# Kernel tuning notes

Measured on AMD Instinct MI355X. Metric: run time of the kernel, lower is better.

The kernel has to match this reference:

```python
import jax, jax.numpy as jnp
import numpy as np

DIM = 1024
NUM_HEADS = 16
HEAD_DIM = DIM // NUM_HEADS
EPS = 1e-5


def layernorm(x, scale, bias):
    # LayerNorm over the last (head_dim) axis
    mu = jnp.mean(x, axis=-1, keepdims=True)
    var = jnp.var(x, axis=-1, keepdims=True)
    return (x - mu) * jax.lax.rsqrt(var + EPS) * scale + bias


def rope(q):
    # q: [B, H, S, Hd]; standard rotate-half RoPE over head_dim
    S, Hd = q.shape[-2], q.shape[-1]
    inv_freq = 1.0 / (10000.0 ** (jnp.arange(0, Hd, 2, dtype=jnp.float32) / Hd))
    ang = jnp.arange(S, dtype=jnp.float32)[:, None] * inv_freq  # [S, Hd/2]
    cos, sin = jnp.cos(ang), jnp.sin(ang)
    q1, q2 = jnp.split(q, 2, axis=-1)
    return jnp.concatenate([q1 * cos - q2 * sin, q1 * sin + q2 * cos], axis=-1)


def setup_inputs() -> dict:
    key = jax.random.key(0)
    ks = jax.random.split(key, 8)
    B, S, S_ctx = 4, 2048, 2048
    s = 0.02
    return {
        "x": jax.random.normal(ks[0], (B, S, DIM), dtype=jnp.float32),
        "context": jax.random.normal(ks[1], (B, S_ctx, DIM), dtype=jnp.float32),
        "q_w": jax.random.normal(ks[2], (DIM, DIM), dtype=jnp.float32) * s,
        "kv_w": jax.random.normal(ks[3], (DIM, 2 * DIM), dtype=jnp.float32) * s,
        "qn_scale": jnp.ones((HEAD_DIM,), jnp.float32),
        "qn_bias": jnp.zeros((HEAD_DIM,), jnp.float32),
        "kn_scale": jnp.ones((HEAD_DIM,), jnp.float32),
        "kn_bias": jnp.zeros((HEAD_DIM,), jnp.float32),
        "proj_w": jax.random.normal(ks[4], (DIM, DIM), dtype=jnp.float32) * s,
        "proj_b": jnp.zeros((DIM,), jnp.float32),
    }


def reference(x, context, q_w, kv_w, qn_scale, qn_bias, kn_scale, kn_bias, proj_w, proj_b):
    B, S, C = x.shape
    S_ctx = context.shape[1]
    H, Hd = NUM_HEADS, HEAD_DIM
    # projections (no bias: qkv_bias=False)
    q = (x @ q_w).reshape(B, S, H, Hd).transpose(0, 2, 1, 3)        # [B,H,S,Hd]
    kv = (context @ kv_w).reshape(B, S_ctx, 2, H, Hd)
    k = kv[:, :, 0].transpose(0, 2, 1, 3)                           # [B,H,Sc,Hd]
    v = kv[:, :, 1].transpose(0, 2, 1, 3)
    # per-head LayerNorm on q and k
    q = layernorm(q, qn_scale, qn_bias)
    k = layernorm(k, kn_scale, kn_bias)
    # RoPE on q only (as in the original forward)
    q = rope(q)
    # SDPA (eval path: no mask, no dropout)
    scale = 1.0 / jnp.sqrt(jnp.float32(Hd))
    logits = jnp.einsum("bhsd,bhtd->bhst", q, k) * scale
    attn = jax.nn.softmax(logits, axis=-1)
    out = jnp.einsum("bhst,bhtd->bhsd", attn, v)                    # [B,H,S,Hd]
    out = out.transpose(0, 2, 1, 3).reshape(B, S, C)
    return out @ proj_w + proj_b
```

## Files before the change

kernel.cpp:

```cpp
#include <hip/hip_runtime.h>
#include <hip/hip_bf16.h>


typedef short bf16x8 __attribute__((ext_vector_type(8)));
typedef float f32x4 __attribute__((ext_vector_type(4)));

__device__ __forceinline__ short f2s(float f) {
    __hip_bfloat16 h = __float2bfloat16(f);
    return __builtin_bit_cast(short, h);
}

__device__ __forceinline__ f32x4 mfma16(bf16x8 a, bf16x8 b, f32x4 c) {
    return __builtin_amdgcn_mfma_f32_16x16x32_bf16(a, b, c, 0, 0, 0);
}

__device__ __forceinline__ void gload16(short* lds, const short* g) {
    __builtin_amdgcn_global_load_lds((const __attribute__((address_space(1))) void*)g,
                                     (__attribute__((address_space(3))) void*)lds,
                                     16, 0, 0);
}

__device__ __forceinline__ void drain_barrier() {
    asm volatile("s_waitcnt vmcnt(0) lgkmcnt(0)" ::: "memory");
    __syncthreads();
}

__device__ __forceinline__ unsigned int fbits(float f) {
    return __builtin_bit_cast(unsigned int, f);
}

__global__ __launch_bounds__(256) void conv_to_bf16(const float* __restrict__ x,
                                                    const float* __restrict__ ctx,
                                                    short* __restrict__ xb,
                                                    short* __restrict__ cb) {
    const size_t NV = 2097152;
    size_t i = (size_t)blockIdx.x * 256 + threadIdx.x;
    const float4* src = (i < NV) ? (const float4*)x : (const float4*)ctx;
    short* dst = (i < NV) ? xb : cb;
    size_t idx = (i < NV) ? i : i - NV;
    float4 v = src[idx];
    short4 o;
    o.x = f2s(v.x); o.y = f2s(v.y); o.z = f2s(v.z); o.w = f2s(v.w);
    ((short4*)dst)[idx] = o;
}

__global__ __launch_bounds__(256) void transpose_weights(
    const float* __restrict__ q_w, const float* __restrict__ kv_w,
    const float* __restrict__ proj_w,
    short* __restrict__ WqT, short* __restrict__ WkvT, short* __restrict__ WpT) {
    __shared__ float t[32][33];
    const float* src; short* dst; int ld, coff;
    switch (blockIdx.z) {
        case 0:  src = q_w;    dst = WqT;                 ld = 1024; coff = 0;    break;
        case 1:  src = kv_w;   dst = WkvT;                ld = 2048; coff = 0;    break;
        case 2:  src = kv_w;   dst = WkvT + 1024 * 1024;  ld = 2048; coff = 1024; break;
        default: src = proj_w; dst = WpT;                 ld = 1024; coff = 0;    break;
    }
    int n0 = blockIdx.x * 32, k0 = blockIdx.y * 32;
    int tx = threadIdx.x & 31, ty = threadIdx.x >> 5;
    #pragma unroll
    for (int j = 0; j < 32; j += 8)
        t[ty + j][tx] = src[(size_t)(k0 + ty + j) * ld + coff + n0 + tx];
    __syncthreads();
    #pragma unroll
    for (int j = 0; j < 32; j += 8)
        dst[(size_t)(n0 + ty + j) * 1024 + k0 + tx] = f2s(t[tx][ty + j]);
}

__global__ __launch_bounds__(256, 3) void gemm_qkv(
    const short* __restrict__ A,
    const short* __restrict__ Bt,
    const short* __restrict__ A2,
    const short* __restrict__ Bt2,
    const float* __restrict__ qn_scale, const float* __restrict__ qn_bias,
    const float* __restrict__ kn_scale, const float* __restrict__ kn_bias,
    short* __restrict__ outQ, short* __restrict__ outK, short* __restrict__ outV) {
    __shared__ short smem[24576];
    const int tid = threadIdx.x;
    const int w = tid >> 6, lane = tid & 63, quad = lane >> 4, l15 = lane & 15;
    const int wr = w & 1, wc = w >> 1;
    const int m0 = blockIdx.x * 128;

    const int y = blockIdx.y;
    const bool qpath = (y < 8);
    const int n0 = qpath ? y * 128 : (y - 8) * 128;
    const short* Ab = qpath ? A : A2;
    const short* Bb = qpath ? Bt : Bt2;
    const float* lns = qpath ? qn_scale : kn_scale;
    const float* lnb = qpath ? qn_bias : kn_bias;
    const bool vpath = (!qpath) && (n0 >= 1024);

    const int srow = lane >> 2, slot = lane & 3;
    const int kslot = (slot ^ ((srow >> 1) & 3)) * 8;
    const short* Ag0 = Ab + (size_t)(m0 + w * 32 + srow) * 1024 + kslot;
    const short* Ag1 = Ag0 + (size_t)16 * 1024;
    const short* Bg0 = Bb + (size_t)(n0 + w * 32 + srow) * 1024 + kslot;
    const short* Bg1 = Bg0 + (size_t)16 * 1024;
    short* Al = smem + w * 1024;
    short* Bl = smem + 4096 + w * 1024;

    f32x4 acc[4][4];
    #pragma unroll
    for (int r = 0; r < 4; r++)
        #pragma unroll
        for (int c = 0; c < 4; c++) acc[r][c] = f32x4{0.f, 0.f, 0.f, 0.f};

    const int rsw = (l15 >> 1) & 3;
    const int rch = (quad ^ rsw) * 8;

    gload16(Al,              Ag0);
    gload16(Al + 512,        Ag1);
    gload16(Bl,              Bg0);
    gload16(Bl + 512,        Bg1);
    gload16(Al + 8192,       Ag0 + 32);
    gload16(Al + 8192 + 512, Ag1 + 32);
    gload16(Bl + 8192,       Bg0 + 32);
    gload16(Bl + 8192 + 512, Bg1 + 32);
    asm volatile("s_waitcnt vmcnt(4) lgkmcnt(0)" ::: "memory");
    __builtin_amdgcn_s_barrier();

    int curo = 0;
    int pfo = 16384;
    #pragma unroll 1
    for (int t = 0; t < 32; t++) {
        if (t < 30) {
            const int k0 = (t + 2) * 32;
            gload16(Al + pfo,       Ag0 + k0);
            gload16(Al + pfo + 512, Ag1 + k0);
            gload16(Bl + pfo,       Bg0 + k0);
            gload16(Bl + pfo + 512, Bg1 + k0);
        }
        bf16x8 af[4], bfr[4];
        #pragma unroll
        for (int rt = 0; rt < 4; rt++)
            af[rt] = *(const bf16x8*)(smem + curo + (wr * 64 + rt * 16 + l15) * 32 + rch);
        #pragma unroll
        for (int ct = 0; ct < 4; ct++)
            bfr[ct] = *(const bf16x8*)(smem + curo + 4096 + (wc * 64 + ct * 16 + l15) * 32 + rch);
        #pragma unroll
        for (int rt = 0; rt < 4; rt++)
            #pragma unroll
            for (int ct = 0; ct < 4; ct++)
                acc[rt][ct] = mfma16(af[rt], bfr[ct], acc[rt][ct]);
        if (t < 30) {
            asm volatile("s_waitcnt vmcnt(4) lgkmcnt(0)" ::: "memory");
        } else {
            asm volatile("s_waitcnt vmcnt(0) lgkmcnt(0)" ::: "memory");
        }
        __builtin_amdgcn_s_barrier();
        curo += 8192; if (curo == 24576) curo = 0;
        pfo  += 8192; if (pfo  == 24576) pfo  = 0;
    }

    if (!vpath) {
        #pragma unroll
        for (int rt = 0; rt < 4; rt++) {
            #pragma unroll
            for (int i = 0; i < 4; i++) {
                float s = acc[rt][0][i] + acc[rt][1][i] + acc[rt][2][i] + acc[rt][3][i];
                float q = acc[rt][0][i] * acc[rt][0][i] + acc[rt][1][i] * acc[rt][1][i] +
                          acc[rt][2][i] * acc[rt][2][i] + acc[rt][3][i] * acc[rt][3][i];
                #pragma unroll
                for (int off = 1; off < 16; off <<= 1) {
                    s += __shfl_xor(s, off, 64);
                    q += __shfl_xor(q, off, 64);
                }
                float mu = s * (1.f / 64.f);
                float var = q * (1.f / 64.f) - mu * mu;
                float rs = rsqrtf(var + 1e-5f);
                float vals[4];
                #pragma unroll
                for (int ct = 0; ct < 4; ct++) {
                    int hd = ct * 16 + l15;
                    vals[ct] = (acc[rt][ct][i] - mu) * rs * lns[hd] + lnb[hd];
                }
                if (qpath) {
                    int sp = (m0 + wr * 64 + rt * 16 + quad * 4 + i) & 2047;
                    #pragma unroll
                    for (int ct = 0; ct < 2; ct++) {
                        int hd1 = ct * 16 + l15;
                        float ang = (float)sp * exp2f((float)hd1 * (-13.287712379549449f / 32.f));
                        float sn, cs;
                        sincosf(ang, &sn, &cs);
                        float v1 = vals[ct], v2 = vals[ct + 2];
                        vals[ct]     = v1 * cs - v2 * sn;
                        vals[ct + 2] = v1 * sn + v2 * cs;
                    }
                    #pragma unroll
                    for (int ct = 0; ct < 4; ct++) vals[ct] *= 0.1803368801f;
                }
                #pragma unroll
                for (int ct = 0; ct < 4; ct++) acc[rt][ct][i] = vals[ct];
            }
        }
        drain_barrier();
        short* Csm = smem;
        #pragma unroll
        for (int rt = 0; rt < 4; rt++)
            #pragma unroll
            for (int ct = 0; ct < 4; ct++)
                #pragma unroll
                for (int i = 0; i < 4; i++)
                    Csm[(wr * 64 + rt * 16 + quad * 4 + i) * 132 + wc * 64 + ct * 16 + l15] =
                        f2s(acc[rt][ct][i]);
        drain_barrier();
        short* dst = qpath ? outQ : outK;
        #pragma unroll
        for (int it = 0; it < 8; it++) {
            int row = it * 16 + (tid >> 4);
            int chunk = tid & 15;
            bf16x8 v = *(const bf16x8*)(Csm + row * 132 + chunk * 8);
            int hh = ((n0 & 1023) >> 6) + (chunk >> 3);
            int m = m0 + row, b = m >> 11, sp = m & 2047;
            *(bf16x8*)(dst + ((size_t)(b * 16 + hh) * 2048 + sp) * 64 + (chunk & 7) * 8) = v;
        }
    } else {
        const int b = m0 >> 11, h = ((n0 - 1024) >> 6) + wc;
        const int sp = (m0 & 2047) + wr * 64 + quad * 4;
        #pragma unroll
        for (int rt = 0; rt < 4; rt++)
            #pragma unroll
            for (int ct = 0; ct < 4; ct++) {
                short4 pk;
                pk.x = f2s(acc[rt][ct][0]); pk.y = f2s(acc[rt][ct][1]);
                pk.z = f2s(acc[rt][ct][2]); pk.w = f2s(acc[rt][ct][3]);
                int hd = ct * 16 + l15;
                *(short4*)(outV + ((size_t)(b * 16 + h) * 64 + hd) * 2048 + sp + rt * 16) = pk;
            }
    }
}

__global__ __launch_bounds__(256, 4) void gemm_proj(
    const short* __restrict__ A,
    const short* __restrict__ Bt,
    float* __restrict__ outF,
    const float* __restrict__ bias_vec) {
    __shared__ short smem[18432];
    const int tid = threadIdx.x;
    const int w = tid >> 6, lane = tid & 63, quad = lane >> 4, l15 = lane & 15;
    const int wr = w & 1, wc = w >> 1;
    const int m0 = blockIdx.x * 64, n0 = blockIdx.y * 128;

    const int srow = lane >> 2, slot = lane & 3;
    const int kslot = (slot ^ ((srow >> 1) & 3)) * 8;
    const short* Ag0 = A + (size_t)(m0 + w * 16 + srow) * 1024 + kslot;
    const short* Bg0 = Bt + (size_t)(n0 + w * 32 + srow) * 1024 + kslot;
    const short* Bg1 = Bg0 + (size_t)16 * 1024;
    short* Al = smem + w * 512;
    short* Bl = smem + 2048 + w * 1024;

    f32x4 acc[2][4];
    #pragma unroll
    for (int r = 0; r < 2; r++)
        #pragma unroll
        for (int c = 0; c < 4; c++) acc[r][c] = f32x4{0.f, 0.f, 0.f, 0.f};

    const int rsw = (l15 >> 1) & 3;
    const int rch = (quad ^ rsw) * 8;

    gload16(Al,              Ag0);
    gload16(Bl,              Bg0);
    gload16(Bl + 512,        Bg1);
    gload16(Al + 6144,       Ag0 + 32);
    gload16(Bl + 6144,       Bg0 + 32);
    gload16(Bl + 6144 + 512, Bg1 + 32);
    asm volatile("s_waitcnt vmcnt(3) lgkmcnt(0)" ::: "memory");
    __builtin_amdgcn_s_barrier();

    int curo = 0;
    int pfo = 12288;
    #pragma unroll 1
    for (int t = 0; t < 32; t++) {
        if (t < 30) {
            const int k0 = (t + 2) * 32;
            gload16(Al + pfo,       Ag0 + k0);
            gload16(Bl + pfo,       Bg0 + k0);
            gload16(Bl + pfo + 512, Bg1 + k0);
        }
        bf16x8 af[2], bfr[4];
        #pragma unroll
        for (int rt = 0; rt < 2; rt++)
            af[rt] = *(const bf16x8*)(smem + curo + (wr * 32 + rt * 16 + l15) * 32 + rch);
        #pragma unroll
        for (int ct = 0; ct < 4; ct++)
            bfr[ct] = *(const bf16x8*)(smem + curo + 2048 + (wc * 64 + ct * 16 + l15) * 32 + rch);
        #pragma unroll
        for (int rt = 0; rt < 2; rt++)
            #pragma unroll
            for (int ct = 0; ct < 4; ct++)
                acc[rt][ct] = mfma16(af[rt], bfr[ct], acc[rt][ct]);
        if (t < 30) {
            asm volatile("s_waitcnt vmcnt(3) lgkmcnt(0)" ::: "memory");
        } else {
            asm volatile("s_waitcnt vmcnt(0) lgkmcnt(0)" ::: "memory");
        }
        __builtin_amdgcn_s_barrier();
        curo += 6144; if (curo == 18432) curo = 0;
        pfo  += 6144; if (pfo  == 18432) pfo  = 0;
    }

    #pragma unroll
    for (int rt = 0; rt < 2; rt++)
        #pragma unroll
        for (int i = 0; i < 4; i++) {
            size_t m = m0 + wr * 32 + rt * 16 + quad * 4 + i;
            #pragma unroll
            for (int ct = 0; ct < 4; ct++) {
                int n = n0 + wc * 64 + ct * 16 + l15;
                outF[m * 1024 + n] = acc[rt][ct][i] + bias_vec[n];
            }
        }
}

__global__ __launch_bounds__(512, 4) void attn_kernel(
    const short* __restrict__ Q,
    const short* __restrict__ K,
    const short* __restrict__ V,
    short* __restrict__ AO) {
    __shared__ short smem[8192 + 8192 + 8 * 32 * 72];
    const int tid = threadIdx.x;
    const int w = tid >> 6, lane = tid & 63, quad = lane >> 4, l15 = lane & 15;
    const int bh = blockIdx.x, qt = blockIdx.y;
    const short* Qb = Q + (size_t)bh * 2048 * 64;
    const short* Kb = K + (size_t)bh * 2048 * 64;
    const short* Vb = V + (size_t)bh * 64 * 2048;
    short* Pw = smem + 16384 + w * 2304;
    const int q0 = qt * 256 + w * 32;

    const int srow = lane >> 2, slot = lane & 3;
    const int sw = (slot ^ ((srow >> 1) & 3)) * 8;
    const int ws = w & 3;
    const bool kstager = (w < 4);
    const short* Sg = kstager ? (Kb + (size_t)(ws * 16 + srow) * 64 + sw)
                              : (Vb + (size_t)(ws * 16 + srow) * 2048 + sw);
    short* Sl0 = smem + (kstager ? 0 : 8192) + ws * 512;
    const int sstep = kstager ? 4096 : 64;

    bf16x8 bq[2][2];
    #pragma unroll
    for (int nt = 0; nt < 2; nt++)
        #pragma unroll
        for (int ks = 0; ks < 2; ks++)
            bq[nt][ks] = *(const bf16x8*)(Qb + (size_t)(q0 + nt * 16 + l15) * 64 + ks * 32 + quad * 8);

    f32x4 acco[4][2];
    #pragma unroll
    for (int ct = 0; ct < 4; ct++)
        #pragma unroll
        for (int nt = 0; nt < 2; nt++) acco[ct][nt] = f32x4{0.f, 0.f, 0.f, 0.f};
    float lsum[2] = {0.f, 0.f};
    const int rsw = (l15 >> 1) & 3;
    const int rch = (quad ^ rsw) * 8;

    gload16(Sl0,        Sg);
    gload16(Sl0 + 2048, Sg + 32);
    drain_barrier();

    #pragma unroll 1
    for (int t = 0; t < 32; t++) {
        const int cur = (t & 1) * 4096;
        if (t < 31) {
            const int nxt = 4096 - cur;
            gload16(Sl0 + nxt,        Sg + (t + 1) * sstep);
            gload16(Sl0 + nxt + 2048, Sg + (t + 1) * sstep + 32);
        }
        bf16x8 ak[4][2];
        #pragma unroll
        for (int mt = 0; mt < 4; mt++)
            #pragma unroll
            for (int ks = 0; ks < 2; ks++)
                ak[mt][ks] = *(const bf16x8*)(smem + cur + ks * 2048 + (mt * 16 + l15) * 32 + rch);

        #pragma unroll
        for (int mt = 0; mt < 4; mt++) {
            #pragma unroll
            for (int nt = 0; nt < 2; nt++) {
                f32x4 st = f32x4{0.f, 0.f, 0.f, 0.f};
                st = mfma16(ak[mt][0], bq[nt][0], st);
                st = mfma16(ak[mt][1], bq[nt][1], st);
                float e0 = __builtin_amdgcn_exp2f(st[0]);
                float e1 = __builtin_amdgcn_exp2f(st[1]);
                float e2 = __builtin_amdgcn_exp2f(st[2]);
                float e3 = __builtin_amdgcn_exp2f(st[3]);
                lsum[nt] += (e0 + e1) + (e2 + e3);
                unsigned int p01 = __builtin_amdgcn_perm(fbits(e1), fbits(e0), 0x07060302u);
                unsigned int p23 = __builtin_amdgcn_perm(fbits(e3), fbits(e2), 0x07060302u);
                uint2 pw;
                pw.x = p01; pw.y = p23;
                *(uint2*)(Pw + (nt * 16 + l15) * 72 + mt * 16 + quad * 4) = pw;
            }
        }
        asm volatile("" ::: "memory");

        bf16x8 av[4][2];
        #pragma unroll
        for (int ct = 0; ct < 4; ct++)
            #pragma unroll
            for (int ks = 0; ks < 2; ks++)
                av[ct][ks] = *(const bf16x8*)(smem + 8192 + cur + ks * 2048 + (ct * 16 + l15) * 32 + rch);

        bf16x8 bp[2][2];
        #pragma unroll
        for (int nt = 0; nt < 2; nt++)
            #pragma unroll
            for (int ks = 0; ks < 2; ks++)
                bp[nt][ks] = *(const bf16x8*)(Pw + (nt * 16 + l15) * 72 + ks * 32 + quad * 8);
        #pragma unroll
        for (int ct = 0; ct < 4; ct++)
            #pragma unroll
            for (int nt = 0; nt < 2; nt++)
                #pragma unroll
                for (int ks = 0; ks < 2; ks++)
                    acco[ct][nt] = mfma16(av[ct][ks], bp[nt][ks], acco[ct][nt]);
        drain_barrier();
    }

    #pragma unroll
    for (int nt = 0; nt < 2; nt++) {
        lsum[nt] += __shfl_xor(lsum[nt], 16, 64);
        lsum[nt] += __shfl_xor(lsum[nt], 32, 64);
    }
    const int b = bh >> 4, h = bh & 15;
    #pragma unroll
    for (int nt = 0; nt < 2; nt++) {
        float inv = 1.f / lsum[nt];
        int sq = q0 + nt * 16 + l15;
        #pragma unroll
        for (int ct = 0; ct < 4; ct++) {
            short4 pk;
            pk.x = f2s(acco[ct][nt][0] * inv); pk.y = f2s(acco[ct][nt][1] * inv);
            pk.z = f2s(acco[ct][nt][2] * inv); pk.w = f2s(acco[ct][nt][3] * inv);
            *(short4*)(AO + ((size_t)b * 2048 + sq) * 1024 + h * 64 + ct * 16 + quad * 4) = pk;
        }
    }
}

extern "C" void kernel_launch(void* const* d_in, const int* in_sizes, int n_in,
                              void* d_out, int out_size, void* d_ws, size_t ws_size,
                              hipStream_t stream) {
    (void)in_sizes; (void)n_in; (void)out_size; (void)ws_size;
    const float* x      = (const float*)d_in[0];
    const float* ctx    = (const float*)d_in[1];
    const float* q_w    = (const float*)d_in[2];
    const float* kv_w   = (const float*)d_in[3];
    const float* qn_s   = (const float*)d_in[4];
    const float* qn_b   = (const float*)d_in[5];
    const float* kn_s   = (const float*)d_in[6];
    const float* kn_b   = (const float*)d_in[7];
    const float* proj_w = (const float*)d_in[8];
    const float* proj_b = (const float*)d_in[9];
    float* out = (float*)d_out;

    char* ws = (char*)d_ws;
    const size_t MB = 1024 * 1024;
    short* xb   = (short*)(ws + 0 * MB);
    short* cb   = (short*)(ws + 16 * MB);
    short* Qb   = (short*)(ws + 32 * MB);
    short* Kb   = (short*)(ws + 48 * MB);
    short* Vt   = (short*)(ws + 64 * MB);
    short* AO   = (short*)(ws + 80 * MB);
    short* WqT  = (short*)(ws + 96 * MB);
    short* WkvT = (short*)(ws + 98 * MB);
    short* WpT  = (short*)(ws + 102 * MB);

    conv_to_bf16<<<16384, 256, 0, stream>>>(x, ctx, xb, cb);
    transpose_weights<<<dim3(32, 32, 4), 256, 0, stream>>>(q_w, kv_w, proj_w, WqT, WkvT, WpT);
    gemm_qkv<<<dim3(64, 24), 256, 0, stream>>>(xb, WqT, cb, WkvT, qn_s, qn_b, kn_s, kn_b,
                                               Qb, Kb, Vt);
    attn_kernel<<<dim3(64, 8), 512, 0, stream>>>(Qb, Kb, Vt, AO);
    gemm_proj<<<dim3(128, 8), 256, 0, stream>>>(AO, WpT, out, proj_b);
}
```

Before: 310.3 us.

## Split output projection GEMM over K with larger tiles and separate bias reduction

The output projection GEMM now uses 128x128 tiles with the K dimension split in two across blockIdx.z. Each half writes fp32 partial results into workspace reused from the freed input and QK buffers. A new elementwise kernel then sums the two partials and adds the bias. Larger tiles give more operand reuse per block, but the change adds a full fp32 partial round trip through memory and an extra kernel launch.

After: 323.8 us. +4.4%, slower.

```diff
diff --git a/kernel.cpp b/kernel.cpp
--- a/kernel.cpp
+++ b/kernel.cpp
@@ -230,28 +230,29 @@
     }
 }
 
-__global__ __launch_bounds__(256, 4) void gemm_proj(
+__global__ __launch_bounds__(256, 3) void gemm_proj_sk(
     const short* __restrict__ A,
     const short* __restrict__ Bt,
-    float* __restrict__ outF,
-    const float* __restrict__ bias_vec) {
-    __shared__ short smem[18432];
+    float* __restrict__ partial) {
+    __shared__ short smem[24576];
     const int tid = threadIdx.x;
     const int w = tid >> 6, lane = tid & 63, quad = lane >> 4, l15 = lane & 15;
     const int wr = w & 1, wc = w >> 1;
-    const int m0 = blockIdx.x * 64, n0 = blockIdx.y * 128;
+    const int m0 = blockIdx.x * 128, n0 = blockIdx.y * 128;
+    const int kz = blockIdx.z;
 
     const int srow = lane >> 2, slot = lane & 3;
     const int kslot = (slot ^ ((srow >> 1) & 3)) * 8;
-    const short* Ag0 = A + (size_t)(m0 + w * 16 + srow) * 1024 + kslot;
-    const short* Bg0 = Bt + (size_t)(n0 + w * 32 + srow) * 1024 + kslot;
+    const short* Ag0 = A + (size_t)(m0 + w * 32 + srow) * 1024 + kz * 512 + kslot;
+    const short* Ag1 = Ag0 + (size_t)16 * 1024;
+    const short* Bg0 = Bt + (size_t)(n0 + w * 32 + srow) * 1024 + kz * 512 + kslot;
     const short* Bg1 = Bg0 + (size_t)16 * 1024;
-    short* Al = smem + w * 512;
-    short* Bl = smem + 2048 + w * 1024;
-
-    f32x4 acc[2][4];
-    #pragma unroll
-    for (int r = 0; r < 2; r++)
+    short* Al = smem + w * 1024;
+    short* Bl = smem + 4096 + w * 1024;
+
+    f32x4 acc[4][4];
+    #pragma unroll
+    for (int r = 0; r < 4; r++)
         #pragma unroll
         for (int c = 0; c < 4; c++) acc[r][c] = f32x4{0.f, 0.f, 0.f, 0.f};
 
@@ -259,57 +260,74 @@
     const int rch = (quad ^ rsw) * 8;
 
     gload16(Al,              Ag0);
+    gload16(Al + 512,        Ag1);
     gload16(Bl,              Bg0);
     gload16(Bl + 512,        Bg1);
-    gload16(Al + 6144,       Ag0 + 32);
-    gload16(Bl + 6144,       Bg0 + 32);
-    gload16(Bl + 6144 + 512, Bg1 + 32);
-    asm volatile("s_waitcnt vmcnt(3) lgkmcnt(0)" ::: "memory");
+    gload16(Al + 8192,       Ag0 + 32);
+    gload16(Al + 8192 + 512, Ag1 + 32);
+    gload16(Bl + 8192,       Bg0 + 32);
+    gload16(Bl + 8192 + 512, Bg1 + 32);
+    asm volatile("s_waitcnt vmcnt(4) lgkmcnt(0)" ::: "memory");
     __builtin_amdgcn_s_barrier();
 
     int curo = 0;
-    int pfo = 12288;
+    int pfo = 16384;
     #pragma unroll 1
-    for (int t = 0; t < 32; t++) {
-        if (t < 30) {
+    for (int t = 0; t < 16; t++) {
+        if (t < 14) {
             const int k0 = (t + 2) * 32;
             gload16(Al + pfo,       Ag0 + k0);
+            gload16(Al + pfo + 512, Ag1 + k0);
             gload16(Bl + pfo,       Bg0 + k0);
             gload16(Bl + pfo + 512, Bg1 + k0);
         }
-        bf16x8 af[2], bfr[4];
-        #pragma unroll
-        for (int rt = 0; rt < 2; rt++)
-            af[rt] = *(const bf16x8*)(smem + curo + (wr * 32 + rt * 16 + l15) * 32 + rch);
+        bf16x8 af[4], bfr[4];
+        #pragma unroll
+        for (int rt = 0; rt < 4; rt++)
+            af[rt] = *(const bf16x8*)(smem + curo + (wr * 64 + rt * 16 + l15) * 32 + rch);
         #pragma unroll
         for (int ct = 0; ct < 4; ct++)
-            bfr[ct] = *(const bf16x8*)(smem + curo + 2048 + (wc * 64 + ct * 16 + l15) * 32 + rch);
-        #pragma unroll
-        for (int rt = 0; rt < 2; rt++)
+            bfr[ct] = *(const bf16x8*)(smem + curo + 4096 + (wc * 64 + ct * 16 + l15) * 32 + rch);
+        #pragma unroll
+        for (int rt = 0; rt < 4; rt++)
             #pragma unroll
             for (int ct = 0; ct < 4; ct++)
                 acc[rt][ct] = mfma16(af[rt], bfr[ct], acc[rt][ct]);
-        if (t < 30) {
-            asm volatile("s_waitcnt vmcnt(3) lgkmcnt(0)" ::: "memory");
+        if (t < 14) {
+            asm volatile("s_waitcnt vmcnt(4) lgkmcnt(0)" ::: "memory");
         } else {
             asm volatile("s_waitcnt vmcnt(0) lgkmcnt(0)" ::: "memory");
         }
         __builtin_amdgcn_s_barrier();
-        curo += 6144; if (curo == 18432) curo = 0;
-        pfo  += 6144; if (pfo  == 18432) pfo  = 0;
-    }
-
-    #pragma unroll
-    for (int rt = 0; rt < 2; rt++)
+        curo += 8192; if (curo == 24576) curo = 0;
+        pfo  += 8192; if (pfo  == 24576) pfo  = 0;
+    }
+
+    float* outP = partial + (size_t)kz * 8192 * 1024;
+    #pragma unroll
+    for (int rt = 0; rt < 4; rt++)
         #pragma unroll
         for (int i = 0; i < 4; i++) {
-            size_t m = m0 + wr * 32 + rt * 16 + quad * 4 + i;
+            size_t m = m0 + wr * 64 + rt * 16 + quad * 4 + i;
             #pragma unroll
             for (int ct = 0; ct < 4; ct++) {
                 int n = n0 + wc * 64 + ct * 16 + l15;
-                outF[m * 1024 + n] = acc[rt][ct][i] + bias_vec[n];
+                outP[m * 1024 + n] = acc[rt][ct][i];
             }
         }
+}
+
+__global__ __launch_bounds__(256) void reduce_bias(
+    const float* __restrict__ partial, const float* __restrict__ bias,
+    float* __restrict__ out) {
+    size_t i = (size_t)blockIdx.x * 256 + threadIdx.x;
+    float4 a = ((const float4*)partial)[i];
+    float4 b = ((const float4*)(partial + (size_t)8192 * 1024))[i];
+    float4 bs = ((const float4*)bias)[i & 255];
+    float4 o;
+    o.x = a.x + b.x + bs.x; o.y = a.y + b.y + bs.y;
+    o.z = a.z + b.z + bs.z; o.w = a.w + b.w + bs.w;
+    ((float4*)out)[i] = o;
 }
 
 __global__ __launch_bounds__(512, 4) void attn_kernel(
@@ -462,11 +480,13 @@
     short* WqT  = (short*)(ws + 96 * MB);
     short* WkvT = (short*)(ws + 98 * MB);
     short* WpT  = (short*)(ws + 102 * MB);
+    float* Pp   = (float*)(ws + 0 * MB);
 
     conv_to_bf16<<<16384, 256, 0, stream>>>(x, ctx, xb, cb);
     transpose_weights<<<dim3(32, 32, 4), 256, 0, stream>>>(q_w, kv_w, proj_w, WqT, WkvT, WpT);
     gemm_qkv<<<dim3(64, 24), 256, 0, stream>>>(xb, WqT, cb, WkvT, qn_s, qn_b, kn_s, kn_b,
                                                Qb, Kb, Vt);
     attn_kernel<<<dim3(64, 8), 512, 0, stream>>>(Qb, Kb, Vt, AO);
-    gemm_proj<<<dim3(128, 8), 256, 0, stream>>>(AO, WpT, out, proj_b);
-}
+    gemm_proj_sk<<<dim3(64, 8, 2), 256, 0, stream>>>(AO, WpT, Pp);
+    reduce_bias<<<8192, 256, 0, stream>>>(Pp, proj_b, out);
+}
```
